# Kernel tuning notes

Measured on AMD Instinct MI355X. Metric: run time of the kernel, lower is better.

The kernel has to match this reference:

```python
import jax, jax.numpy as jnp
import numpy as np

EPS = 1e-6

def _rmsnorm(x, w):
    var = jnp.mean(x * x, axis=-1, keepdims=True)
    return w * (x * jax.lax.rsqrt(var + EPS))

def _rope(t, cos, sin):
    # t: [B,S,H,d_k]; cos/sin: [S,d_k/2] -> complex multiply on (even,odd) pairs
    B, S, H, D = t.shape
    tr = t.reshape(B, S, H, D // 2, 2)
    t0, t1 = tr[..., 0], tr[..., 1]
    c = cos[None, :, None, :]
    s = sin[None, :, None, :]
    o0 = t0 * c - t1 * s
    o1 = t0 * s + t1 * c
    return jnp.stack([o0, o1], axis=-1).reshape(B, S, H, D)

def setup_inputs() -> dict:
    key = jax.random.key(0)
    ks = jax.random.split(key, 9)
    B, S, D, H, DFF = 1, 4096, 1024, 16, 4096
    dk = D // H
    hidden = int(2 * DFF / 3)  # 2730, SwiGLU hidden dim
    sc = 0.02
    x = jax.random.normal(ks[0], (B, S, D), jnp.float32)
    # RoPE tables (theta=10000)
    inv_freq = 1.0 / (10000.0 ** (np.arange(0, dk, 2, dtype=np.float32) / dk))
    ang = np.outer(np.arange(S, dtype=np.float32), inv_freq)
    freqs_cos = jnp.asarray(np.cos(ang))
    freqs_sin = jnp.asarray(np.sin(ang))
    # causal additive mask [1,1,S,S]
    mask = jnp.where(np.tril(np.ones((S, S), bool)), 0.0, -1e9).astype(jnp.float32)[None, None]
    Wq = jax.random.normal(ks[1], (D, D), jnp.float32) * sc
    Wk = jax.random.normal(ks[2], (D, D), jnp.float32) * sc
    Wv = jax.random.normal(ks[3], (D, D), jnp.float32) * sc
    Wo = jax.random.normal(ks[4], (D, D), jnp.float32) * sc
    ln1_w = jnp.ones((D,), jnp.float32)
    ln2_w = jnp.ones((D,), jnp.float32)
    w1 = jax.random.normal(ks[5], (D, hidden), jnp.float32) * sc
    w2 = jax.random.normal(ks[6], (hidden, D), jnp.float32) * sc
    w3 = jax.random.normal(ks[7], (D, hidden), jnp.float32) * sc
    return dict(x=x, freqs_cos=freqs_cos, freqs_sin=freqs_sin, mask=mask,
                Wq=Wq, Wk=Wk, Wv=Wv, Wo=Wo, ln1_w=ln1_w, ln2_w=ln2_w,
                w1=w1, w2=w2, w3=w3)

def reference(x, freqs_cos, freqs_sin, mask, Wq, Wk, Wv, Wo, ln1_w, ln2_w, w1, w2, w3):
    B, S, D = x.shape
    H = 16
    dk = D // H
    scale = jnp.sqrt(jnp.float32(dk))
    # attention sublayer (pre-RMSNorm)
    h = _rmsnorm(x, ln1_w)
    Q = (h @ Wq).reshape(B, S, H, dk)
    K = (h @ Wk).reshape(B, S, H, dk)
    V = (h @ Wv).reshape(B, S, H, dk)
    Q = _rope(Q, freqs_cos, freqs_sin)
    K = _rope(K, freqs_cos, freqs_sin)
    scores = jnp.einsum('bshd,bthd->bhst', Q, K) / scale + mask  # [B,H,S,S]
    attn = jax.nn.softmax(scores, axis=-1)
    ctx = jnp.einsum('bhst,bthd->bshd', attn, V).reshape(B, S, D)
    x = x + ctx @ Wo
    # SwiGLU FFN sublayer
    h2 = _rmsnorm(x, ln2_w)
    ff = (jax.nn.silu(h2 @ w1) * (h2 @ w3)) @ w2
    x = x + ff
    return x
```

## Files before the change

kernel.cpp:

```cpp
#include <hip/hip_runtime.h>

#define S_LEN 4096
#define D_MODEL 1024
#define NHEAD 16
#define DK 64
#define HID 2730
#define HIDP 2816
#define QKV_LD 3072

typedef unsigned short u16;
typedef unsigned int u32;
typedef __bf16 bf16x8 __attribute__((ext_vector_type(8)));
typedef float f32x4 __attribute__((ext_vector_type(4)));

#define MFMA16 __builtin_amdgcn_mfma_f32_16x16x32_bf16

__device__ __forceinline__ float b2f(u16 u) {
    return __builtin_bit_cast(float, (u32)u << 16);
}
__device__ __forceinline__ u16 f2b(float f) {
    u32 u = __builtin_bit_cast(u32, f);
    u += 0x7FFF + ((u >> 16) & 1);
    return (u16)(u >> 16);
}
__device__ __forceinline__ u32 pk_trunc(float lo, float hi) {
    return __builtin_amdgcn_perm(__builtin_bit_cast(u32, hi),
                                 __builtin_bit_cast(u32, lo), 0x07060302u);
}
__device__ __forceinline__ void gll16(const u16* g, u16* l) {
    __builtin_amdgcn_global_load_lds(
        (__attribute__((address_space(1))) void*)(g),
        (__attribute__((address_space(3))) void*)(l),
        16, 0, 0);
}

__global__ __launch_bounds__(256)
void rmsnorm_k(const float* __restrict__ x, const float* __restrict__ w,
               u16* __restrict__ out) {
    const int row = blockIdx.x;
    const int tid = threadIdx.x;
    const float4 v = ((const float4*)(x + (size_t)row * D_MODEL))[tid];
    float ss = v.x * v.x + v.y * v.y + v.z * v.z + v.w * v.w;
    for (int o = 32; o; o >>= 1) ss += __shfl_down(ss, o);
    __shared__ float red[4];
    if ((tid & 63) == 0) red[tid >> 6] = ss;
    __syncthreads();
    const float tot = red[0] + red[1] + red[2] + red[3];
    const float rs = rsqrtf(tot * (1.0f / D_MODEL) + 1e-6f);
    const float4 wv = ((const float4*)w)[tid];
    u16* op = out + (size_t)row * D_MODEL + tid * 4;
    u32 p0 = (u32)f2b(v.x * rs * wv.x) | ((u32)f2b(v.y * rs * wv.y) << 16);
    u32 p1 = (u32)f2b(v.z * rs * wv.z) | ((u32)f2b(v.w * rs * wv.w) << 16);
    uint2 pk; pk.x = p0; pk.y = p1;
    *(uint2*)op = pk;
}

__global__ __launch_bounds__(256)
void tcast_all(const float* s0, const float* s1, const float* s2,
               const float* s3, const float* s4, const float* s5,
               const float* s6, u16* d0, u16* d1, u16* d2, u16* d3,
               u16* d4, u16* d5, u16* d6) {
    const float* srcs[7] = {s0, s1, s2, s3, s4, s5, s6};
    u16* dsts[7] = {d0, d1, d2, d3, d4, d5, d6};
    const int RR[7] = {1024, 1024, 1024, 1024, 1024, 1024, 2730};
    const int CC[7] = {1024, 1024, 1024, 1024, 2730, 2730, 1024};
    const int OC[7] = {1024, 1024, 1024, 1024, 1024, 1024, 2816};
    const int XD[7] = {32, 32, 32, 32, 32, 32, 88};

    const int bid = blockIdx.x;
    int seg, start;
    if (bid < 4096)      { seg = bid >> 10; start = seg << 10; }
    else if (bid < 6912) { seg = 4; start = 4096; }
    else if (bid < 9728) { seg = 5; start = 6912; }
    else                 { seg = 6; start = 9728; }
    const int local = bid - start;
    const int bx = local % XD[seg], byy = local / XD[seg];
    const float* in = srcs[seg];
    u16* out = dsts[seg];
    const int R = RR[seg], C = CC[seg], outC = OC[seg];

    __shared__ float t[32][33];
    const int r0 = byy * 32;
    const int c0 = bx * 32;
    const int tx = threadIdx.x, ty = threadIdx.y;
#pragma unroll
    for (int j = 0; j < 4; ++j) {
        int ir = c0 + ty + j * 8;
        int ic = r0 + tx;
        t[ty + j * 8][tx] = (ir < R && ic < C) ? in[(size_t)ir * C + ic] : 0.0f;
    }
    __syncthreads();
#pragma unroll
    for (int j = 0; j < 4; ++j)
        out[(size_t)(r0 + ty + j * 8) * outC + c0 + tx] = f2b(t[tx][ty + j * 8]);
}

__global__ __launch_bounds__(256)
void packkv_k(const u16* __restrict__ qkv, const float* __restrict__ fc,
              const float* __restrict__ fs, u16* __restrict__ vt,
              u16* __restrict__ kp) {
    __shared__ u16 t[32][33];
    const int h = blockIdx.z;
    const int t0 = blockIdx.x * 32;
    const int d0 = blockIdx.y * 32;
    const int tx = threadIdx.x, ty = threadIdx.y;
#pragma unroll
    for (int j = 0; j < 4; ++j)
        t[ty + j * 8][tx] =
            qkv[(size_t)(t0 + ty + j * 8) * QKV_LD + 2 * D_MODEL + h * DK + d0 + tx];

    const int id = ty * 32 + tx;
    const int sA = t0 + (id >> 3);
    const int dA = d0 + (id & 7) * 4;
    uint2 kvp = *(const uint2*)(qkv + (size_t)sA * QKV_LD + D_MODEL + h * DK + dA);
    const int fi = sA * 32 + (dA >> 1);
    const float cc0 = fc[fi], ss0 = fs[fi];
    const float cc1 = fc[fi + 1], ss1 = fs[fi + 1];
    auto rpk = [](u32 w, float c, float s) -> u32 {
        const float a = b2f((u16)w), b = b2f((u16)(w >> 16));
        return (u32)f2b(a * c - b * s) | ((u32)f2b(a * s + b * c) << 16);
    };
    kvp.x = rpk(kvp.x, cc0, ss0);
    kvp.y = rpk(kvp.y, cc1, ss1);
    *(uint2*)(kp + ((size_t)h * S_LEN + sA) * DK + dA) = kvp;

    __syncthreads();
#pragma unroll
    for (int j = 0; j < 4; ++j)
        vt[(size_t)h * DK * S_LEN + (size_t)(d0 + ty + j * 8) * S_LEN + t0 + tx] =
            t[tx][ty + j * 8];
}

template <int EPI>
__global__ __launch_bounds__(256)
void gemm128(const u16* __restrict__ A, int lda, const u16* __restrict__ Bt, int ldb,
             void* __restrict__ C, int ldc, int K, const float* __restrict__ resid) {
    const int m0 = blockIdx.y * 128, n0 = blockIdx.x * 128;
    const int tid = threadIdx.x;
    const int wave = tid >> 6, lane = tid & 63;
    const int wr = wave >> 1, wc = wave & 1;
    const int r16 = lane & 15, kq = lane >> 4;

    __shared__ __align__(16) u16 As[128 * 32];
    __shared__ __align__(16) u16 Bs[128 * 32];

    const int srow = tid >> 2, sk = (tid & 3) * 8;
    const u16* ag0 = A + (size_t)(m0 + srow) * lda + sk;
    const u16* ag1 = A + (size_t)(m0 + 64 + srow) * lda + sk;
    const u16* bg0 = Bt + (size_t)(n0 + srow) * ldb + sk;
    const u16* bg1 = Bt + (size_t)(n0 + 64 + srow) * ldb + sk;
    u16* asw = As + wave * 512;
    u16* bsw = Bs + wave * 512;

    f32x4 acc[16];
#pragma unroll
    for (int i = 0; i < 16; ++i) acc[i] = f32x4{0.f, 0.f, 0.f, 0.f};

    for (int k0 = 0; k0 < K; k0 += 32) {
        __syncthreads();
        gll16(ag0 + k0, asw);
        gll16(ag1 + k0, asw + 2048);
        gll16(bg0 + k0, bsw);
        gll16(bg1 + k0, bsw + 2048);
        __syncthreads();
        bf16x8 af[4], bf[4];
#pragma unroll
        for (int mt = 0; mt < 4; ++mt)
            af[mt] = *(const bf16x8*)&As[(wr * 64 + mt * 16 + r16) * 32 + kq * 8];
#pragma unroll
        for (int nt = 0; nt < 4; ++nt)
            bf[nt] = *(const bf16x8*)&Bs[(wc * 64 + nt * 16 + r16) * 32 + kq * 8];
#pragma unroll
        for (int mt = 0; mt < 4; ++mt)
#pragma unroll
            for (int nt = 0; nt < 4; ++nt)
                acc[mt * 4 + nt] = MFMA16(af[mt], bf[nt], acc[mt * 4 + nt], 0, 0, 0);
    }

#pragma unroll
    for (int mt = 0; mt < 4; ++mt) {
#pragma unroll
        for (int nt = 0; nt < 4; ++nt) {
            const int col = n0 + wc * 64 + nt * 16 + r16;
#pragma unroll
            for (int j = 0; j < 4; ++j) {
                const int row = m0 + wr * 64 + mt * 16 + kq * 4 + j;
                if (EPI == 0) {
                    ((u16*)C)[(size_t)row * ldc + col] = f2b(acc[mt * 4 + nt][j]);
                } else {
                    ((float*)C)[(size_t)row * ldc + col] =
                        resid[(size_t)row * ldc + col] + acc[mt * 4 + nt][j];
                }
            }
        }
    }
}

__global__ __launch_bounds__(256)
void gemm64r(const u16* __restrict__ A, int lda, const u16* __restrict__ Bt, int ldb,
             float* __restrict__ C, int ldc, int K, const float* __restrict__ resid) {
    const int m0 = blockIdx.y * 128, n0 = blockIdx.x * 64;
    const int tid = threadIdx.x;
    const int wave = tid >> 6, lane = tid & 63;
    const int r16 = lane & 15, kq = lane >> 4;

    __shared__ __align__(16) u16 As[128 * 32];
    __shared__ __align__(16) u16 Bs[64 * 32];

    const int srow = tid >> 2, sk = (tid & 3) * 8;
    const u16* ag0 = A + (size_t)(m0 + srow) * lda + sk;
    const u16* ag1 = A + (size_t)(m0 + 64 + srow) * lda + sk;
    const u16* bg = Bt + (size_t)(n0 + srow) * ldb + sk;
    u16* asw = As + wave * 512;
    u16* bsw = Bs + wave * 512;

    f32x4 acc[8];
#pragma unroll
    for (int i = 0; i < 8; ++i) acc[i] = f32x4{0.f, 0.f, 0.f, 0.f};

    for (int k0 = 0; k0 < K; k0 += 32) {
        __syncthreads();
        gll16(ag0 + k0, asw);
        gll16(ag1 + k0, asw + 2048);
        gll16(bg + k0, bsw);
        __syncthreads();
        bf16x8 af[2], bf[4];
#pragma unroll
        for (int mt = 0; mt < 2; ++mt)
            af[mt] = *(const bf16x8*)&As[(wave * 32 + mt * 16 + r16) * 32 + kq * 8];
#pragma unroll
        for (int nt = 0; nt < 4; ++nt)
            bf[nt] = *(const bf16x8*)&Bs[(nt * 16 + r16) * 32 + kq * 8];
#pragma unroll
        for (int mt = 0; mt < 2; ++mt)
#pragma unroll
            for (int nt = 0; nt < 4; ++nt)
                acc[mt * 4 + nt] = MFMA16(af[mt], bf[nt], acc[mt * 4 + nt], 0, 0, 0);
    }

#pragma unroll
    for (int mt = 0; mt < 2; ++mt)
#pragma unroll
        for (int nt = 0; nt < 4; ++nt) {
            const int col = n0 + nt * 16 + r16;
#pragma unroll
            for (int j = 0; j < 4; ++j) {
                const int row = m0 + wave * 32 + mt * 16 + kq * 4 + j;
                C[(size_t)row * ldc + col] =
                    resid[(size_t)row * ldc + col] + acc[mt * 4 + nt][j];
            }
        }
}

__global__ __launch_bounds__(256)
void gemm_dual64(const u16* __restrict__ A, int lda,
                 const u16* __restrict__ B1, const u16* __restrict__ B3, int ldb,
                 u16* __restrict__ C, int ldc, int K) {
    const int m0 = blockIdx.y * 128, n0 = blockIdx.x * 64;
    const int tid = threadIdx.x;
    const int wave = tid >> 6, lane = tid & 63;
    const int r16 = lane & 15, kq = lane >> 4;

    __shared__ __align__(16) u16 As[128 * 32];
    __shared__ __align__(16) u16 B1s[64 * 32];
    __shared__ __align__(16) u16 B3s[64 * 32];

    const int srow = tid >> 2, sk = (tid & 3) * 8;
    const u16* ag0 = A + (size_t)(m0 + srow) * lda + sk;
    const u16* ag1 = A + (size_t)(m0 + 64 + srow) * lda + sk;
    const u16* b1g = B1 + (size_t)(n0 + srow) * ldb + sk;
    const u16* b3g = B3 + (size_t)(n0 + srow) * ldb + sk;
    u16* asw = As + wave * 512;
    u16* b1w = B1s + wave * 512;
    u16* b3w = B3s + wave * 512;

    f32x4 acc1[8], acc3[8];
#pragma unroll
    for (int i = 0; i < 8; ++i) {
        acc1[i] = f32x4{0.f, 0.f, 0.f, 0.f};
        acc3[i] = f32x4{0.f, 0.f, 0.f, 0.f};
    }

    for (int k0 = 0; k0 < K; k0 += 32) {
        __syncthreads();
        gll16(ag0 + k0, asw);
        gll16(ag1 + k0, asw + 2048);
        gll16(b1g + k0, b1w);
        gll16(b3g + k0, b3w);
        __syncthreads();
        bf16x8 af[2], b1f[4], b3f[4];
#pragma unroll
        for (int mt = 0; mt < 2; ++mt)
            af[mt] = *(const bf16x8*)&As[(wave * 32 + mt * 16 + r16) * 32 + kq * 8];
#pragma unroll
        for (int nt = 0; nt < 4; ++nt) {
            b1f[nt] = *(const bf16x8*)&B1s[(nt * 16 + r16) * 32 + kq * 8];
            b3f[nt] = *(const bf16x8*)&B3s[(nt * 16 + r16) * 32 + kq * 8];
        }
#pragma unroll
        for (int mt = 0; mt < 2; ++mt)
#pragma unroll
            for (int nt = 0; nt < 4; ++nt) {
                acc1[mt * 4 + nt] = MFMA16(af[mt], b1f[nt], acc1[mt * 4 + nt], 0, 0, 0);
                acc3[mt * 4 + nt] = MFMA16(af[mt], b3f[nt], acc3[mt * 4 + nt], 0, 0, 0);
            }
    }

#pragma unroll
    for (int mt = 0; mt < 2; ++mt)
#pragma unroll
        for (int nt = 0; nt < 4; ++nt) {
            const int col = n0 + nt * 16 + r16;
#pragma unroll
            for (int j = 0; j < 4; ++j) {
                const int row = m0 + wave * 32 + mt * 16 + kq * 4 + j;
                const float v1 = acc1[mt * 4 + nt][j];
                const float v3 = acc3[mt * 4 + nt][j];
                const float sig = 1.0f / (1.0f + __expf(-v1));
                C[(size_t)row * ldc + col] = f2b(v1 * sig * v3);
            }
        }
}

__global__ __launch_bounds__(256)
void flash_k(const u16* __restrict__ qkv, const u16* __restrict__ vt,
             const u16* __restrict__ kp, const float* __restrict__ fc,
             const float* __restrict__ fs, u16* __restrict__ ctx) {
    const int h = blockIdx.x;
    const int by = blockIdx.y;
    const int hi = by >> 4, lo = by & 15;
    const int base = lo + ((hi >> 1) << 4);
    const int qi = (hi & 1) ? (63 - base) : base;
    const int q0 = qi * 64;
    const int tid = threadIdx.x;
    const int wave = tid >> 6, lane = tid & 63;
    const int r16 = lane & 15, kq = lane >> 4;

    __shared__ __align__(16) u16 KsA[64 * 64];
    __shared__ __align__(16) u16 KsB[64 * 64];
    __shared__ __align__(16) u16 VsA[64 * 64];
    __shared__ __align__(16) u16 VsB[64 * 64];
    __shared__ __align__(16) u16 Ps[4 * 16 * 64];

    const u16* kb = kp + (size_t)h * S_LEN * DK;
    const u16* vb = vt + (size_t)h * DK * S_LEN;
    const int srow = tid >> 3;
    const int lcol = ((tid & 7) ^ (srow & 7)) * 8;
    const int qloc = wave * 16 + r16;
    const int qglob = q0 + qloc;
    const int sw = r16 & 7;
    const int c0 = (kq ^ sw) * 8;
    const int c1 = ((4 ^ kq) ^ sw) * 8;
    const int psw = r16 & 14;
    u16* psrow = Ps + wave * 1024 + r16 * 64;

    const float SC = 0.125f * 1.44269504f;
    const u16* qrow = qkv + (size_t)qglob * QKV_LD + h * DK;
    uint4 uq0 = *(const uint4*)(qrow + kq * 8);
    uint4 uq1 = *(const uint4*)(qrow + 32 + kq * 8);
    const float4 c0v = *(const float4*)(fc + qglob * 32 + kq * 4);
    const float4 s0v = *(const float4*)(fs + qglob * 32 + kq * 4);
    const float4 c1v = *(const float4*)(fc + qglob * 32 + 16 + kq * 4);
    const float4 s1v = *(const float4*)(fs + qglob * 32 + 16 + kq * 4);
    auto rp = [SC](u32 w, float c, float s) -> u32 {
        const float a = b2f((u16)w), b = b2f((u16)(w >> 16));
        return (u32)f2b((a * c - b * s) * SC) |
               ((u32)f2b((a * s + b * c) * SC) << 16);
    };
    uq0.x = rp(uq0.x, c0v.x, s0v.x); uq0.y = rp(uq0.y, c0v.y, s0v.y);
    uq0.z = rp(uq0.z, c0v.z, s0v.z); uq0.w = rp(uq0.w, c0v.w, s0v.w);
    uq1.x = rp(uq1.x, c1v.x, s1v.x); uq1.y = rp(uq1.y, c1v.y, s1v.y);
    uq1.z = rp(uq1.z, c1v.z, s1v.z); uq1.w = rp(uq1.w, c1v.w, s1v.w);
    const bf16x8 qf0 = __builtin_bit_cast(bf16x8, uq0);
    const bf16x8 qf1 = __builtin_bit_cast(bf16x8, uq1);

    f32x4 o[4];
#pragma unroll
    for (int i = 0; i < 4; ++i) o[i] = f32x4{0.f, 0.f, 0.f, 0.f};
    float lpart = 0.f;
    const int T = (qi + 2) >> 1;

    for (int t = 0; t < T; ++t) {
        const int t0 = t * 128;
        __syncthreads();
#pragma unroll
        for (int i = 0; i < 2; ++i) {
            const int r = srow + i * 32;
            gll16(kb + (size_t)(t0 + r) * DK + lcol, KsA + tid * 8 + i * 2048);
            gll16(kb + (size_t)(t0 + 64 + r) * DK + lcol, KsB + tid * 8 + i * 2048);
            gll16(vb + (size_t)r * S_LEN + t0 + lcol, VsA + tid * 8 + i * 2048);
            gll16(vb + (size_t)r * S_LEN + t0 + 64 + lcol, VsB + tid * 8 + i * 2048);
        }
        __syncthreads();

        f32x4 s[8];
#pragma unroll
        for (int nt = 0; nt < 4; ++nt) {
            s[nt] = f32x4{0.f, 0.f, 0.f, 0.f};
            const bf16x8 k0 = *(const bf16x8*)&KsA[(nt * 16 + r16) * 64 + c0];
            s[nt] = MFMA16(k0, qf0, s[nt], 0, 0, 0);
            const bf16x8 k1 = *(const bf16x8*)&KsA[(nt * 16 + r16) * 64 + c1];
            s[nt] = MFMA16(k1, qf1, s[nt], 0, 0, 0);
        }
#pragma unroll
        for (int nt = 0; nt < 4; ++nt) {
            s[4 + nt] = f32x4{0.f, 0.f, 0.f, 0.f};
            const bf16x8 k0 = *(const bf16x8*)&KsB[(nt * 16 + r16) * 64 + c0];
            s[4 + nt] = MFMA16(k0, qf0, s[4 + nt], 0, 0, 0);
            const bf16x8 k1 = *(const bf16x8*)&KsB[(nt * 16 + r16) * 64 + c1];
            s[4 + nt] = MFMA16(k1, qf1, s[4 + nt], 0, 0, 0);
        }

        const bool lastT = (t == T - 1);
#pragma unroll
        for (int p = 0; p < 2; ++p) {
            float pr[16];
#pragma unroll
            for (int nt = 0; nt < 4; ++nt)
#pragma unroll
                for (int j = 0; j < 4; ++j)
                    pr[nt * 4 + j] = exp2f(s[p * 4 + nt][j]);
            if (lastT) {
                const int kvb = t0 + p * 64;
#pragma unroll
                for (int nt = 0; nt < 4; ++nt)
#pragma unroll
                    for (int j = 0; j < 4; ++j)
                        if ((kvb + nt * 16 + kq * 4 + j) > qglob)
                            pr[nt * 4 + j] = 0.f;
            }
#pragma unroll
            for (int i = 0; i < 16; ++i) lpart += pr[i];

#pragma unroll
            for (int nt = 0; nt < 4; ++nt) {
                uint2 pk;
                pk.x = pk_trunc(pr[nt * 4 + 0], pr[nt * 4 + 1]);
                pk.y = pk_trunc(pr[nt * 4 + 2], pr[nt * 4 + 3]);
                *(uint2*)&psrow[((nt * 4 + kq) ^ psw) * 4] = pk;
            }

#pragma unroll
            for (int ks = 0; ks < 2; ++ks) {
                const bf16x8 pf =
                    *(const bf16x8*)&psrow[((8 * ks + 2 * kq) ^ psw) * 4];
                const int cv = (((ks << 2) ^ kq) ^ sw) * 8;
#pragma unroll
                for (int nt = 0; nt < 4; ++nt) {
                    const bf16x8 vf = p
                        ? *(const bf16x8*)&VsB[(nt * 16 + r16) * 64 + cv]
                        : *(const bf16x8*)&VsA[(nt * 16 + r16) * 64 + cv];
                    o[nt] = MFMA16(vf, pf, o[nt], 0, 0, 0);
                }
            }
        }
    }

    lpart += __shfl_xor(lpart, 16);
    lpart += __shfl_xor(lpart, 32);
    const float inv = 1.0f / lpart;
    const size_t row = qglob;
#pragma unroll
    for (int nt = 0; nt < 4; ++nt) {
        uint2 pk;
        pk.x = (u32)f2b(o[nt][0] * inv) | ((u32)f2b(o[nt][1] * inv) << 16);
        pk.y = (u32)f2b(o[nt][2] * inv) | ((u32)f2b(o[nt][3] * inv) << 16);
        *(uint2*)&ctx[row * D_MODEL + h * DK + nt * 16 + kq * 4] = pk;
    }
}

extern "C" void kernel_launch(void* const* d_in, const int* in_sizes, int n_in,
                              void* d_out, int out_size, void* d_ws, size_t ws_size,
                              hipStream_t stream) {
    const float* x    = (const float*)d_in[0];
    const float* fcos = (const float*)d_in[1];
    const float* fsin = (const float*)d_in[2];
    const float* Wq = (const float*)d_in[4];
    const float* Wk = (const float*)d_in[5];
    const float* Wv = (const float*)d_in[6];
    const float* Wo = (const float*)d_in[7];
    const float* ln1 = (const float*)d_in[8];
    const float* ln2 = (const float*)d_in[9];
    const float* w1 = (const float*)d_in[10];
    const float* w2 = (const float*)d_in[11];
    const float* w3 = (const float*)d_in[12];
    float* out = (float*)d_out;

    char* ws = (char*)d_ws;
    size_t off = 0;
    auto alloc = [&](size_t bytes) -> char* {
        char* p = ws + off;
        off += (bytes + 255) & ~(size_t)255;
        return p;
    };
    u16* hb    = (u16*)alloc((size_t)S_LEN * D_MODEL * 2);
    u16* wqkvt = (u16*)alloc((size_t)QKV_LD * D_MODEL * 2);
    u16* wot   = (u16*)alloc((size_t)D_MODEL * D_MODEL * 2);
    u16* qkvb  = (u16*)alloc((size_t)S_LEN * QKV_LD * 2);
    u16* vt    = (u16*)alloc((size_t)S_LEN * D_MODEL * 2);
    u16* kpack = (u16*)alloc((size_t)S_LEN * D_MODEL * 2);
    u16* ctxb  = (u16*)alloc((size_t)S_LEN * D_MODEL * 2);
    float* x2  = (float*)alloc((size_t)S_LEN * D_MODEL * 4);
    u16* h2b   = (u16*)alloc((size_t)S_LEN * D_MODEL * 2);
    u16* w1t   = (u16*)alloc((size_t)HIDP * D_MODEL * 2);
    u16* w3t   = (u16*)alloc((size_t)HIDP * D_MODEL * 2);
    u16* w2t   = (u16*)alloc((size_t)D_MODEL * HIDP * 2);
    u16* ffb   = (u16*)alloc((size_t)S_LEN * HIDP * 2);

    const dim3 tb32(32, 8);

    tcast_all<<<12544, tb32, 0, stream>>>(
        Wq, Wk, Wv, Wo, w1, w3, w2,
        wqkvt, wqkvt + (size_t)D_MODEL * D_MODEL,
        wqkvt + (size_t)2 * D_MODEL * D_MODEL, wot, w1t, w3t, w2t);

    rmsnorm_k<<<S_LEN, 256, 0, stream>>>(x, ln1, hb);

    gemm128<0><<<dim3(QKV_LD / 128, S_LEN / 128), 256, 0, stream>>>(
        hb, D_MODEL, wqkvt, D_MODEL, qkvb, QKV_LD, D_MODEL, nullptr);

    packkv_k<<<dim3(S_LEN / 32, DK / 32, NHEAD), tb32, 0, stream>>>(
        qkvb, fcos, fsin, vt, kpack);

    flash_k<<<dim3(NHEAD, 64), 256, 0, stream>>>(qkvb, vt, kpack, fcos, fsin, ctxb);

    gemm64r<<<dim3(D_MODEL / 64, S_LEN / 128), 256, 0, stream>>>(
        ctxb, D_MODEL, wot, D_MODEL, x2, D_MODEL, D_MODEL, x);

    rmsnorm_k<<<S_LEN, 256, 0, stream>>>(x2, ln2, h2b);

    gemm_dual64<<<dim3(HIDP / 64, S_LEN / 128), 256, 0, stream>>>(
        h2b, D_MODEL, w1t, w3t, D_MODEL, ffb, HIDP, D_MODEL);

    gemm64r<<<dim3(D_MODEL / 64, S_LEN / 128), 256, 0, stream>>>(
        ffb, HIDP, w2t, HIDP, out, D_MODEL, HIDP, x2);
}
```

Before: 424.2 us.

## Double-buffer flash K/V tiles, compute row sums via MFMA, fuse prep kernels

The flash attention loop now walks 64-wide KV tiles and prefetches the next tile into a second LDS buffer while the current one is computed, with one barrier per iteration instead of two. This is meant to hide global load latency. The softmax denominator is now taken with an MFMA against a ones vector instead of scalar adds followed by cross-lane shuffles, so it sums the bf16-truncated probabilities. The weight transpose-cast kernel and the first RMSNorm are merged into a single launch to save one kernel launch.

```diff
diff --git a/kernel.cpp b/kernel.cpp
--- a/kernel.cpp
+++ b/kernel.cpp
@@ -32,6 +32,69 @@
         (__attribute__((address_space(1))) void*)(g),
         (__attribute__((address_space(3))) void*)(l),
         16, 0, 0);
+}
+
+__global__ __launch_bounds__(256)
+void prep_k(const float* s0, const float* s1, const float* s2,
+            const float* s3, const float* s4, const float* s5,
+            const float* s6, u16* d0, u16* d1, u16* d2, u16* d3,
+            u16* d4, u16* d5, u16* d6,
+            const float* __restrict__ x, const float* __restrict__ ln1,
+            u16* __restrict__ hb) {
+    __shared__ float t[32][33];
+    __shared__ float red[4];
+    const int bid = blockIdx.x;
+    const int tid = threadIdx.x;
+
+    if (bid >= 12544) {
+        const int row = bid - 12544;
+        const float4 v = ((const float4*)(x + (size_t)row * D_MODEL))[tid];
+        float ss = v.x * v.x + v.y * v.y + v.z * v.z + v.w * v.w;
+        for (int o = 32; o; o >>= 1) ss += __shfl_down(ss, o);
+        if ((tid & 63) == 0) red[tid >> 6] = ss;
+        __syncthreads();
+        const float tot = red[0] + red[1] + red[2] + red[3];
+        const float rs = rsqrtf(tot * (1.0f / D_MODEL) + 1e-6f);
+        const float4 wv = ((const float4*)ln1)[tid];
+        u16* op = hb + (size_t)row * D_MODEL + tid * 4;
+        u32 p0 = (u32)f2b(v.x * rs * wv.x) | ((u32)f2b(v.y * rs * wv.y) << 16);
+        u32 p1 = (u32)f2b(v.z * rs * wv.z) | ((u32)f2b(v.w * rs * wv.w) << 16);
+        uint2 pk; pk.x = p0; pk.y = p1;
+        *(uint2*)op = pk;
+        return;
+    }
+
+    const float* srcs[7] = {s0, s1, s2, s3, s4, s5, s6};
+    u16* dsts[7] = {d0, d1, d2, d3, d4, d5, d6};
+    const int RR[7] = {1024, 1024, 1024, 1024, 1024, 1024, 2730};
+    const int CC[7] = {1024, 1024, 1024, 1024, 2730, 2730, 1024};
+    const int OC[7] = {1024, 1024, 1024, 1024, 1024, 1024, 2816};
+    const int XD[7] = {32, 32, 32, 32, 32, 32, 88};
+
+    int seg, start;
+    if (bid < 4096)      { seg = bid >> 10; start = seg << 10; }
+    else if (bid < 6912) { seg = 4; start = 4096; }
+    else if (bid < 9728) { seg = 5; start = 6912; }
+    else                 { seg = 6; start = 9728; }
+    const int local = bid - start;
+    const int bx = local % XD[seg], byy = local / XD[seg];
+    const float* in = srcs[seg];
+    u16* out = dsts[seg];
+    const int R = RR[seg], C = CC[seg], outC = OC[seg];
+
+    const int r0 = byy * 32;
+    const int c0 = bx * 32;
+    const int tx = tid & 31, ty = tid >> 5;
+#pragma unroll
+    for (int j = 0; j < 4; ++j) {
+        int ir = c0 + ty + j * 8;
+        int ic = r0 + tx;
+        t[ty + j * 8][tx] = (ir < R && ic < C) ? in[(size_t)ir * C + ic] : 0.0f;
+    }
+    __syncthreads();
+#pragma unroll
+    for (int j = 0; j < 4; ++j)
+        out[(size_t)(r0 + ty + j * 8) * outC + c0 + tx] = f2b(t[tx][ty + j * 8]);
 }
 
 __global__ __launch_bounds__(256)
@@ -56,46 +119,6 @@
 }
 
 __global__ __launch_bounds__(256)
-void tcast_all(const float* s0, const float* s1, const float* s2,
-               const float* s3, const float* s4, const float* s5,
-               const float* s6, u16* d0, u16* d1, u16* d2, u16* d3,
-               u16* d4, u16* d5, u16* d6) {
-    const float* srcs[7] = {s0, s1, s2, s3, s4, s5, s6};
-    u16* dsts[7] = {d0, d1, d2, d3, d4, d5, d6};
-    const int RR[7] = {1024, 1024, 1024, 1024, 1024, 1024, 2730};
-    const int CC[7] = {1024, 1024, 1024, 1024, 2730, 2730, 1024};
-    const int OC[7] = {1024, 1024, 1024, 1024, 1024, 1024, 2816};
-    const int XD[7] = {32, 32, 32, 32, 32, 32, 88};
-
-    const int bid = blockIdx.x;
-    int seg, start;
-    if (bid < 4096)      { seg = bid >> 10; start = seg << 10; }
-    else if (bid < 6912) { seg = 4; start = 4096; }
-    else if (bid < 9728) { seg = 5; start = 6912; }
-    else                 { seg = 6; start = 9728; }
-    const int local = bid - start;
-    const int bx = local % XD[seg], byy = local / XD[seg];
-    const float* in = srcs[seg];
-    u16* out = dsts[seg];
-    const int R = RR[seg], C = CC[seg], outC = OC[seg];
-
-    __shared__ float t[32][33];
-    const int r0 = byy * 32;
-    const int c0 = bx * 32;
-    const int tx = threadIdx.x, ty = threadIdx.y;
-#pragma unroll
-    for (int j = 0; j < 4; ++j) {
-        int ir = c0 + ty + j * 8;
-        int ic = r0 + tx;
-        t[ty + j * 8][tx] = (ir < R && ic < C) ? in[(size_t)ir * C + ic] : 0.0f;
-    }
-    __syncthreads();
-#pragma unroll
-    for (int j = 0; j < 4; ++j)
-        out[(size_t)(r0 + ty + j * 8) * outC + c0 + tx] = f2b(t[tx][ty + j * 8]);
-}
-
-__global__ __launch_bounds__(256)
 void packkv_k(const u16* __restrict__ qkv, const float* __restrict__ fc,
               const float* __restrict__ fs, u16* __restrict__ vt,
               u16* __restrict__ kp) {
@@ -336,10 +359,8 @@
     const int wave = tid >> 6, lane = tid & 63;
     const int r16 = lane & 15, kq = lane >> 4;
 
-    __shared__ __align__(16) u16 KsA[64 * 64];
-    __shared__ __align__(16) u16 KsB[64 * 64];
-    __shared__ __align__(16) u16 VsA[64 * 64];
-    __shared__ __align__(16) u16 VsB[64 * 64];
+    __shared__ __align__(16) u16 Kb[2][64 * 64];
+    __shared__ __align__(16) u16 Vb[2][64 * 64];
     __shared__ __align__(16) u16 Ps[4 * 16 * 64];
 
     const u16* kb = kp + (size_t)h * S_LEN * DK;
@@ -377,88 +398,78 @@
     f32x4 o[4];
 #pragma unroll
     for (int i = 0; i < 4; ++i) o[i] = f32x4{0.f, 0.f, 0.f, 0.f};
-    float lpart = 0.f;
-    const int T = (qi + 2) >> 1;
-
-    for (int t = 0; t < T; ++t) {
-        const int t0 = t * 128;
-        __syncthreads();
-#pragma unroll
-        for (int i = 0; i < 2; ++i) {
-            const int r = srow + i * 32;
-            gll16(kb + (size_t)(t0 + r) * DK + lcol, KsA + tid * 8 + i * 2048);
-            gll16(kb + (size_t)(t0 + 64 + r) * DK + lcol, KsB + tid * 8 + i * 2048);
-            gll16(vb + (size_t)r * S_LEN + t0 + lcol, VsA + tid * 8 + i * 2048);
-            gll16(vb + (size_t)r * S_LEN + t0 + 64 + lcol, VsB + tid * 8 + i * 2048);
-        }
-        __syncthreads();
-
-        f32x4 s[8];
+    f32x4 lacc = f32x4{0.f, 0.f, 0.f, 0.f};
+    const uint4 uone = make_uint4(0x3F803F80u, 0x3F803F80u, 0x3F803F80u, 0x3F803F80u);
+    const bf16x8 ones = __builtin_bit_cast(bf16x8, uone);
+
+#pragma unroll
+    for (int i = 0; i < 2; ++i) {
+        const int r = srow + i * 32;
+        gll16(kb + (size_t)r * DK + lcol, Kb[0] + tid * 8 + i * 2048);
+        gll16(vb + (size_t)r * S_LEN + lcol, Vb[0] + tid * 8 + i * 2048);
+    }
+
+    for (int t = 0; t <= qi; ++t) {
+        __syncthreads();
+        if (t < qi) {
+            const int t1 = (t + 1) * 64;
+            u16* kd = Kb[(t + 1) & 1];
+            u16* vd = Vb[(t + 1) & 1];
+#pragma unroll
+            for (int i = 0; i < 2; ++i) {
+                const int r = srow + i * 32;
+                gll16(kb + (size_t)(t1 + r) * DK + lcol, kd + tid * 8 + i * 2048);
+                gll16(vb + (size_t)r * S_LEN + t1 + lcol, vd + tid * 8 + i * 2048);
+            }
+        }
+        const u16* Ks = Kb[t & 1];
+        const u16* Vs = Vb[t & 1];
+
+        f32x4 s[4];
 #pragma unroll
         for (int nt = 0; nt < 4; ++nt) {
             s[nt] = f32x4{0.f, 0.f, 0.f, 0.f};
-            const bf16x8 k0 = *(const bf16x8*)&KsA[(nt * 16 + r16) * 64 + c0];
+            const bf16x8 k0 = *(const bf16x8*)&Ks[(nt * 16 + r16) * 64 + c0];
             s[nt] = MFMA16(k0, qf0, s[nt], 0, 0, 0);
-            const bf16x8 k1 = *(const bf16x8*)&KsA[(nt * 16 + r16) * 64 + c1];
+            const bf16x8 k1 = *(const bf16x8*)&Ks[(nt * 16 + r16) * 64 + c1];
             s[nt] = MFMA16(k1, qf1, s[nt], 0, 0, 0);
         }
+
+        float pr[16];
+#pragma unroll
+        for (int nt = 0; nt < 4; ++nt)
+#pragma unroll
+            for (int j = 0; j < 4; ++j) pr[nt * 4 + j] = exp2f(s[nt][j]);
+        if (t == qi) {
+#pragma unroll
+            for (int nt = 0; nt < 4; ++nt)
+#pragma unroll
+                for (int j = 0; j < 4; ++j)
+                    if ((nt * 16 + kq * 4 + j) > qloc) pr[nt * 4 + j] = 0.f;
+        }
+
 #pragma unroll
         for (int nt = 0; nt < 4; ++nt) {
-            s[4 + nt] = f32x4{0.f, 0.f, 0.f, 0.f};
-            const bf16x8 k0 = *(const bf16x8*)&KsB[(nt * 16 + r16) * 64 + c0];
-            s[4 + nt] = MFMA16(k0, qf0, s[4 + nt], 0, 0, 0);
-            const bf16x8 k1 = *(const bf16x8*)&KsB[(nt * 16 + r16) * 64 + c1];
-            s[4 + nt] = MFMA16(k1, qf1, s[4 + nt], 0, 0, 0);
-        }
-
-        const bool lastT = (t == T - 1);
-#pragma unroll
-        for (int p = 0; p < 2; ++p) {
-            float pr[16];
-#pragma unroll
-            for (int nt = 0; nt < 4; ++nt)
-#pragma unroll
-                for (int j = 0; j < 4; ++j)
-                    pr[nt * 4 + j] = exp2f(s[p * 4 + nt][j]);
-            if (lastT) {
-                const int kvb = t0 + p * 64;
-#pragma unroll
-                for (int nt = 0; nt < 4; ++nt)
-#pragma unroll
-                    for (int j = 0; j < 4; ++j)
-                        if ((kvb + nt * 16 + kq * 4 + j) > qglob)
-                            pr[nt * 4 + j] = 0.f;
+            uint2 pk;
+            pk.x = pk_trunc(pr[nt * 4 + 0], pr[nt * 4 + 1]);
+            pk.y = pk_trunc(pr[nt * 4 + 2], pr[nt * 4 + 3]);
+            *(uint2*)&psrow[((nt * 4 + kq) ^ psw) * 4] = pk;
+        }
+
+#pragma unroll
+        for (int ks = 0; ks < 2; ++ks) {
+            const bf16x8 pf = *(const bf16x8*)&psrow[((8 * ks + 2 * kq) ^ psw) * 4];
+            lacc = MFMA16(ones, pf, lacc, 0, 0, 0);
+            const int cv = (((ks << 2) ^ kq) ^ sw) * 8;
+#pragma unroll
+            for (int nt = 0; nt < 4; ++nt) {
+                const bf16x8 vf = *(const bf16x8*)&Vs[(nt * 16 + r16) * 64 + cv];
+                o[nt] = MFMA16(vf, pf, o[nt], 0, 0, 0);
             }
-#pragma unroll
-            for (int i = 0; i < 16; ++i) lpart += pr[i];
-
-#pragma unroll
-            for (int nt = 0; nt < 4; ++nt) {
-                uint2 pk;
-                pk.x = pk_trunc(pr[nt * 4 + 0], pr[nt * 4 + 1]);
-                pk.y = pk_trunc(pr[nt * 4 + 2], pr[nt * 4 + 3]);
-                *(uint2*)&psrow[((nt * 4 + kq) ^ psw) * 4] = pk;
-            }
-
-#pragma unroll
-            for (int ks = 0; ks < 2; ++ks) {
-                const bf16x8 pf =
-                    *(const bf16x8*)&psrow[((8 * ks + 2 * kq) ^ psw) * 4];
-                const int cv = (((ks << 2) ^ kq) ^ sw) * 8;
-#pragma unroll
-                for (int nt = 0; nt < 4; ++nt) {
-                    const bf16x8 vf = p
-                        ? *(const bf16x8*)&VsB[(nt * 16 + r16) * 64 + cv]
-                        : *(const bf16x8*)&VsA[(nt * 16 + r16) * 64 + cv];
-                    o[nt] = MFMA16(vf, pf, o[nt], 0, 0, 0);
-                }
-            }
-        }
-    }
-
-    lpart += __shfl_xor(lpart, 16);
-    lpart += __shfl_xor(lpart, 32);
-    const float inv = 1.0f / lpart;
+        }
+    }
+
+    const float inv = 1.0f / lacc[0];
     const size_t row = qglob;
 #pragma unroll
     for (int nt = 0; nt < 4; ++nt) {
@@ -509,12 +520,11 @@
 
     const dim3 tb32(32, 8);
 
-    tcast_all<<<12544, tb32, 0, stream>>>(
+    prep_k<<<16640, 256, 0, stream>>>(
         Wq, Wk, Wv, Wo, w1, w3, w2,
         wqkvt, wqkvt + (size_t)D_MODEL * D_MODEL,
-        wqkvt + (size_t)2 * D_MODEL * D_MODEL, wot, w1t, w3t, w2t);
-
-    rmsnorm_k<<<S_LEN, 256, 0, stream>>>(x, ln1, hb);
+        wqkvt + (size_t)2 * D_MODEL * D_MODEL, wot, w1t, w3t, w2t,
+        x, ln1, hb);
 
     gemm128<0><<<dim3(QKV_LD / 128, S_LEN / 128), 256, 0, stream>>>(
         hb, D_MODEL, wqkvt, D_MODEL, qkvb, QKV_LD, D_MODEL, nullptr);
```

New measurement: 423.1 us. Within noise of the previous version (-0.3%).
